# Kernel optimization log

Measured on AMD Instinct MI355X. Metric: run time of the kernel, lower is better.

Reference implementation:

```python
import jax, jax.numpy as jnp
import numpy as np

B, T, C = 256, 512, 256
K = 8  # number of distinct phoneme classes used (indices into phoneme_inventory)
# weights dict {'aa':2.0,'ae':0.5,'ah':1.5,'ao':1.2,'aw':0.8}, rest default 1.0,
# materialized as a dense per-class-index weight vector:
WEIGHTS = np.ones(K, dtype=np.float32)
WEIGHTS[:5] = [2.0, 0.5, 1.5, 1.2, 0.8]


def setup_inputs() -> dict:
    key = jax.random.key(0)
    k1, k2 = jax.random.split(key)
    embeddings = jax.random.normal(k1, (B, T, C), dtype=jnp.float32)
    phonemes = jax.random.randint(k2, (B, T), 0, K, dtype=jnp.int64)
    weights = jnp.asarray(WEIGHTS)
    return {"embeddings": embeddings, "phonemes": phonemes, "weights": weights}


def reference(embeddings, phonemes, weights):
    Bs, Ts, Cs = embeddings.shape
    # F.normalize(p=2, dim=-1) with eps=1e-12
    norm = jnp.linalg.norm(embeddings, axis=-1, keepdims=True)
    emb = embeddings / jnp.maximum(norm, 1e-12)
    # all-pairs cosine similarity per timestep: [T, B, B]
    exp_sim = jnp.exp(jnp.einsum('itc,jtc->tij', emb, emb))
    eye = jnp.eye(Bs, dtype=bool)  # [B, B]
    p = phonemes.T  # [T, B]
    pos = (p[:, :, None] == p[:, None, :]) & ~eye  # [T, B, B]
    num = jnp.where(pos, exp_sim, 0.0).sum(-1)          # [T, B]
    den = jnp.where(~eye, exp_sim, 0.0).sum(-1)          # [T, B]
    per_sample = -jnp.log(num / (den + 1e-6))            # [T, B]
    # segment-mean per (timestep, class), then weighted mean over present classes
    oh = jax.nn.one_hot(p, weights.shape[0], dtype=per_sample.dtype)  # [T, B, K]
    counts = oh.sum(1)                                   # [T, K]
    sums = jnp.einsum('tb,tbk->tk', per_sample, oh)      # [T, K]
    present = counts > 0
    class_mean = sums / jnp.maximum(counts, 1.0)
    loss_t = jnp.where(present, class_mean * weights, 0.0).sum(-1) / present.sum(-1)
    return loss_t.mean()
```

## Files before the change

### kernel.cpp

```cpp
#include <hip/hip_runtime.h>

#define Bn 256
#define Tn 512
#define Cn 256
#define Kn 8

typedef __attribute__((ext_vector_type(4))) float f32x4;

__global__ __launch_bounds__(512, 4)
void tcon_k(const float* __restrict__ emb,
            const int* __restrict__ phon,
            const float* __restrict__ wts,
            float* __restrict__ out) {
    __shared__ __align__(16) unsigned char Esh[Bn * Bn];
    __shared__ float invn[Bn];
    __shared__ int   pcls[Bn];
    __shared__ float num_s[Bn], den_s[Bn];
    __shared__ float csum[Kn];
    __shared__ int   ccnt[Kn];

    const int t    = blockIdx.x;
    const int tid  = threadIdx.x;
    const int lane = tid & 63;
    const int wave = tid >> 6;
    const int i0   = wave * 32;

    const int q   = lane >> 4;
    const int l15 = lane & 15;
    const int e3  = l15 & 7;

    if (tid < Kn) { csum[tid] = 0.0f; ccnt[tid] = 0; }
    if (tid < Bn) pcls[tid] = phon[tid * Tn + t];

    #pragma unroll 4
    for (int it = 0; it < 16; ++it) {
        const int f   = tid + it * 512;
        const int row = f >> 5;
        const int b   = f & 31;
        const float4* p = (const float4*)(emb + ((size_t)row * Tn + t) * Cn);
        const float4 v0 = p[2 * b];
        const float4 v1 = p[2 * b + 1];
        int lo = __builtin_amdgcn_cvt_pk_fp8_f32(v0.x, v0.y, 0, false);
        lo     = __builtin_amdgcn_cvt_pk_fp8_f32(v0.z, v0.w, lo, true);
        int hi = __builtin_amdgcn_cvt_pk_fp8_f32(v1.x, v1.y, 0, false);
        hi     = __builtin_amdgcn_cvt_pk_fp8_f32(v1.z, v1.w, hi, true);
        const int qq = b & 3, kk = b >> 2, kp = kk >> 1;
        const int ad = row * 256 + ((((qq << 2) + kp) ^ (row & 7)) << 4)
                     + ((kk & 1) << 3);
        int2 pk; pk.x = lo; pk.y = hi;
        *(int2*)&Esh[ad] = pk;
    }
    __syncthreads();

    f32x4 acc[2][2];

#define COMPUTE_HALF(JB) do {                                                \
    _Pragma("unroll") for (int _m = 0; _m < 2; ++_m)                         \
    _Pragma("unroll") for (int _n = 0; _n < 2; ++_n)                         \
        acc[_m][_n] = (f32x4){0.f, 0.f, 0.f, 0.f};                           \
    _Pragma("unroll") for (int _kp = 0; _kp < 4; ++_kp) {                    \
        const int _sw = (((q << 2) + _kp) ^ e3) << 4;                        \
        ulonglong2 _a[2], _b[2];                                             \
        _Pragma("unroll") for (int _m = 0; _m < 2; ++_m)                     \
            _a[_m] = *(const ulonglong2*)&Esh[(i0 + _m * 16 + l15) * 256 + _sw]; \
        _Pragma("unroll") for (int _n = 0; _n < 2; ++_n)                     \
            _b[_n] = *(const ulonglong2*)&Esh[((JB) + _n * 16 + l15) * 256 + _sw]; \
        _Pragma("unroll") for (int _m = 0; _m < 2; ++_m)                     \
        _Pragma("unroll") for (int _n = 0; _n < 2; ++_n) {                   \
            acc[_m][_n] = __builtin_amdgcn_mfma_f32_16x16x32_fp8_fp8(        \
                (long)_a[_m].x, (long)_b[_n].x, acc[_m][_n], 0, 0, 0);       \
            acc[_m][_n] = __builtin_amdgcn_mfma_f32_16x16x32_fp8_fp8(        \
                (long)_a[_m].y, (long)_b[_n].y, acc[_m][_n], 0, 0, 0);       \
        }                                                                    \
    }                                                                        \
} while (0)

#define EPILOGUE(JB) do {                                                    \
    _Pragma("unroll") for (int _n = 0; _n < 2; ++_n) {                       \
        const int _j  = (JB) + _n * 16 + l15;                                \
        const int _pj = pcls[_j];                                            \
        const float _ij = invn[_j];                                          \
        _Pragma("unroll") for (int _m = 0; _m < 2; ++_m)                     \
        _Pragma("unroll") for (int _r = 0; _r < 4; ++_r) {                   \
            const int _e = _m * 4 + _r;                                      \
            const int _ir = i0 + _m * 16 + q * 4 + _r;                       \
            const float _ex = __expf(acc[_m][_n][_r] * inv_i[_e] * _ij);     \
            const bool _nd = (_ir != _j);                                    \
            den_p[_e] += _nd ? _ex : 0.0f;                                   \
            num_p[_e] += (_nd && (_pj == pi[_e])) ? _ex : 0.0f;              \
        }                                                                    \
    }                                                                        \
} while (0)

    COMPUTE_HALF(i0);
    #pragma unroll
    for (int r = 0; r < 4; ++r)
        if (l15 == q * 4 + r) {
            invn[i0 + l15]      = rsqrtf(fmaxf(acc[0][0][r], 1e-24f));
            invn[i0 + 16 + l15] = rsqrtf(fmaxf(acc[1][1][r], 1e-24f));
        }
    __syncthreads();

    float num_p[8], den_p[8], inv_i[8];
    int   pi[8];
    #pragma unroll
    for (int e = 0; e < 8; ++e) {
        const int irow = i0 + (e >> 2) * 16 + q * 4 + (e & 3);
        num_p[e] = 0.0f; den_p[e] = 0.0f;
        pi[e]    = pcls[irow];
        inv_i[e] = invn[irow];
    }

    EPILOGUE(i0);
    for (int k = 1; k < 8; ++k) {
        const int jb = (wave ^ k) * 32;
        COMPUTE_HALF(jb);
        EPILOGUE(jb);
    }

    #pragma unroll
    for (int e = 0; e < 8; ++e) {
        float n = num_p[e], d = den_p[e];
        #pragma unroll
        for (int m = 1; m <= 8; m <<= 1) {
            n += __shfl_xor(n, m, 64);
            d += __shfl_xor(d, m, 64);
        }
        if (l15 == e) {
            const int irow = i0 + (e >> 2) * 16 + q * 4 + (e & 3);
            num_s[irow] = n;
            den_s[irow] = d;
        }
    }
    __syncthreads();

    if (tid < Bn) {
        const float ps = __logf(den_s[tid] + 1e-6f) - __logf(num_s[tid]);
        atomicAdd(&csum[pcls[tid]], ps);
        atomicAdd(&ccnt[pcls[tid]], 1);
    }
    __syncthreads();

    if (tid == 0) {
        float accv = 0.0f; int np = 0;
        #pragma unroll
        for (int k = 0; k < Kn; ++k)
            if (ccnt[k] > 0) { accv += (csum[k] / (float)ccnt[k]) * wts[k]; ++np; }
        atomicAdd(out, (accv / (float)np) * (1.0f / (float)Tn));
    }
#undef COMPUTE_HALF
#undef EPILOGUE
}

extern "C" void kernel_launch(void* const* d_in, const int* in_sizes, int n_in,
                              void* d_out, int out_size, void* d_ws, size_t ws_size,
                              hipStream_t stream) {
    const float* emb  = (const float*)d_in[0];
    const int*   phon = (const int*)d_in[1];
    const float* wts  = (const float*)d_in[2];
    float*       out  = (float*)d_out;

    hipMemsetAsync(out, 0, sizeof(float), stream);
    tcon_k<<<Tn, 512, 0, stream>>>(emb, phon, wts, out);
}
```

Baseline: 207.3 us.

## Use 1024-thread blocks with 16-row wave tiles instead of 32-row

```diff
diff --git a/kernel.cpp b/kernel.cpp
--- a/kernel.cpp
+++ b/kernel.cpp
@@ -7,7 +7,7 @@
 
 typedef __attribute__((ext_vector_type(4))) float f32x4;
 
-__global__ __launch_bounds__(512, 4)
+__global__ __launch_bounds__(1024, 8)
 void tcon_k(const float* __restrict__ emb,
             const int* __restrict__ phon,
             const float* __restrict__ wts,
@@ -23,7 +23,8 @@
     const int tid  = threadIdx.x;
     const int lane = tid & 63;
     const int wave = tid >> 6;
-    const int i0   = wave * 32;
+    const int i0   = wave * 16;
+    const int g0   = wave >> 1;
 
     const int q   = lane >> 4;
     const int l15 = lane & 15;
@@ -33,8 +34,8 @@
     if (tid < Bn) pcls[tid] = phon[tid * Tn + t];
 
     #pragma unroll 4
-    for (int it = 0; it < 16; ++it) {
-        const int f   = tid + it * 512;
+    for (int it = 0; it < 8; ++it) {
+        const int f   = tid + it * 1024;
         const int row = f >> 5;
         const int b   = f & 31;
         const float4* p = (const float4*)(emb + ((size_t)row * Tn + t) * Cn);
@@ -52,25 +53,22 @@
     }
     __syncthreads();
 
-    f32x4 acc[2][2];
+    f32x4 acc[2];
 
-#define COMPUTE_HALF(JB) do {                                                \
-    _Pragma("unroll") for (int _m = 0; _m < 2; ++_m)                         \
-    _Pragma("unroll") for (int _n = 0; _n < 2; ++_n)                         \
-        acc[_m][_n] = (f32x4){0.f, 0.f, 0.f, 0.f};                           \
+#define COMPUTE_G(JB) do {                                                   \
+    acc[0] = (f32x4){0.f, 0.f, 0.f, 0.f};                                    \
+    acc[1] = (f32x4){0.f, 0.f, 0.f, 0.f};                                    \
     _Pragma("unroll") for (int _kp = 0; _kp < 4; ++_kp) {                    \
         const int _sw = (((q << 2) + _kp) ^ e3) << 4;                        \
-        ulonglong2 _a[2], _b[2];                                             \
-        _Pragma("unroll") for (int _m = 0; _m < 2; ++_m)                     \
-            _a[_m] = *(const ulonglong2*)&Esh[(i0 + _m * 16 + l15) * 256 + _sw]; \
+        const ulonglong2 _a = *(const ulonglong2*)&Esh[(i0 + l15) * 256 + _sw]; \
+        ulonglong2 _b[2];                                                    \
         _Pragma("unroll") for (int _n = 0; _n < 2; ++_n)                     \
             _b[_n] = *(const ulonglong2*)&Esh[((JB) + _n * 16 + l15) * 256 + _sw]; \
-        _Pragma("unroll") for (int _m = 0; _m < 2; ++_m)                     \
         _Pragma("unroll") for (int _n = 0; _n < 2; ++_n) {                   \
-            acc[_m][_n] = __builtin_amdgcn_mfma_f32_16x16x32_fp8_fp8(        \
-                (long)_a[_m].x, (long)_b[_n].x, acc[_m][_n], 0, 0, 0);       \
-            acc[_m][_n] = __builtin_amdgcn_mfma_f32_16x16x32_fp8_fp8(        \
-                (long)_a[_m].y, (long)_b[_n].y, acc[_m][_n], 0, 0, 0);       \
+            acc[_n] = __builtin_amdgcn_mfma_f32_16x16x32_fp8_fp8(            \
+                (long)_a.x, (long)_b[_n].x, acc[_n], 0, 0, 0);               \
+            acc[_n] = __builtin_amdgcn_mfma_f32_16x16x32_fp8_fp8(            \
+                (long)_a.y, (long)_b[_n].y, acc[_n], 0, 0, 0);               \
         }                                                                    \
     }                                                                        \
 } while (0)
@@ -80,46 +78,49 @@
         const int _j  = (JB) + _n * 16 + l15;                                \
         const int _pj = pcls[_j];                                            \
         const float _ij = invn[_j];                                          \
-        _Pragma("unroll") for (int _m = 0; _m < 2; ++_m)                     \
         _Pragma("unroll") for (int _r = 0; _r < 4; ++_r) {                   \
-            const int _e = _m * 4 + _r;                                      \
-            const int _ir = i0 + _m * 16 + q * 4 + _r;                       \
-            const float _ex = __expf(acc[_m][_n][_r] * inv_i[_e] * _ij);     \
+            const int _ir = i0 + q * 4 + _r;                                 \
+            const float _ex = __expf(acc[_n][_r] * inv_i[_r] * _ij);         \
             const bool _nd = (_ir != _j);                                    \
-            den_p[_e] += _nd ? _ex : 0.0f;                                   \
-            num_p[_e] += (_nd && (_pj == pi[_e])) ? _ex : 0.0f;              \
+            den_p[_r] += _nd ? _ex : 0.0f;                                   \
+            num_p[_r] += (_nd && (_pj == pi[_r])) ? _ex : 0.0f;              \
         }                                                                    \
     }                                                                        \
 } while (0)
 
-    COMPUTE_HALF(i0);
-    #pragma unroll
-    for (int r = 0; r < 4; ++r)
-        if (l15 == q * 4 + r) {
-            invn[i0 + l15]      = rsqrtf(fmaxf(acc[0][0][r], 1e-24f));
-            invn[i0 + 16 + l15] = rsqrtf(fmaxf(acc[1][1][r], 1e-24f));
-        }
+    COMPUTE_G(g0 * 32);
+    if ((wave & 1) == 0) {
+        #pragma unroll
+        for (int r = 0; r < 4; ++r)
+            if (l15 == q * 4 + r)
+                invn[i0 + l15] = rsqrtf(fmaxf(acc[0][r], 1e-24f));
+    } else {
+        #pragma unroll
+        for (int r = 0; r < 4; ++r)
+            if (l15 == q * 4 + r)
+                invn[i0 + l15] = rsqrtf(fmaxf(acc[1][r], 1e-24f));
+    }
     __syncthreads();
 
-    float num_p[8], den_p[8], inv_i[8];
-    int   pi[8];
+    float num_p[4], den_p[4], inv_i[4];
+    int   pi[4];
     #pragma unroll
-    for (int e = 0; e < 8; ++e) {
-        const int irow = i0 + (e >> 2) * 16 + q * 4 + (e & 3);
+    for (int e = 0; e < 4; ++e) {
+        const int irow = i0 + q * 4 + e;
         num_p[e] = 0.0f; den_p[e] = 0.0f;
         pi[e]    = pcls[irow];
         inv_i[e] = invn[irow];
     }
 
-    EPILOGUE(i0);
+    EPILOGUE(g0 * 32);
     for (int k = 1; k < 8; ++k) {
-        const int jb = (wave ^ k) * 32;
-        COMPUTE_HALF(jb);
+        const int jb = (g0 ^ k) * 32;
+        COMPUTE_G(jb);
         EPILOGUE(jb);
     }
 
     #pragma unroll
-    for (int e = 0; e < 8; ++e) {
+    for (int e = 0; e < 4; ++e) {
         float n = num_p[e], d = den_p[e];
         #pragma unroll
         for (int m = 1; m <= 8; m <<= 1) {
@@ -127,9 +128,8 @@
             d += __shfl_xor(d, m, 64);
         }
         if (l15 == e) {
-            const int irow = i0 + (e >> 2) * 16 + q * 4 + (e & 3);
-            num_s[irow] = n;
-            den_s[irow] = d;
+            num_s[i0 + q * 4 + e] = n;
+            den_s[i0 + q * 4 + e] = d;
         }
     }
     __syncthreads();
@@ -148,7 +148,7 @@
             if (ccnt[k] > 0) { accv += (csum[k] / (float)ccnt[k]) * wts[k]; ++np; }
         atomicAdd(out, (accv / (float)np) * (1.0f / (float)Tn));
     }
-#undef COMPUTE_HALF
+#undef COMPUTE_G
 #undef EPILOGUE
 }
 
@@ -161,5 +161,5 @@
     float*       out  = (float*)d_out;
 
     hipMemsetAsync(out, 0, sizeof(float), stream);
-    tcon_k<<<Tn, 512, 0, stream>>>(emb, phon, wts, out);
+    tcon_k<<<Tn, 1024, 0, stream>>>(emb, phon, wts, out);
 }
```

After: 358.1 us. 1.73x slower.

## Split into prepass that normalizes and packs fp8 tiles, then direct LDS-load matmul kernel

Applied to the files above, without the earlier changes.

```diff
diff --git a/kernel.cpp b/kernel.cpp
--- a/kernel.cpp
+++ b/kernel.cpp
@@ -6,13 +6,167 @@
 #define Kn 8
 
 typedef __attribute__((ext_vector_type(4))) float f32x4;
+typedef __attribute__((address_space(1))) const unsigned char g_u8;
+typedef __attribute__((address_space(3))) unsigned char l_u8;
+
 
 __global__ __launch_bounds__(512, 4)
-void tcon_k(const float* __restrict__ emb,
+void tcon_p(const float* __restrict__ emb, unsigned char* __restrict__ q8) {
+    const int tid  = threadIdx.x;
+    const int lane = tid & 63;
+    const int wave = tid >> 6;
+    const int R    = blockIdx.x * 8 + wave;
+    const int b    = R >> 9;
+    const int t    = R & (Tn - 1);
+
+    const float4 v = ((const float4*)(emb + (size_t)R * Cn))[lane];
+    float n2 = v.x * v.x + v.y * v.y + v.z * v.z + v.w * v.w;
+    #pragma unroll
+    for (int m = 1; m <= 32; m <<= 1) n2 += __shfl_xor(n2, m, 64);
+    const float inv = rsqrtf(fmaxf(n2, 1e-24f));
+
+    int pk = __builtin_amdgcn_cvt_pk_fp8_f32(v.x * inv, v.y * inv, 0, false);
+    pk     = __builtin_amdgcn_cvt_pk_fp8_f32(v.z * inv, v.w * inv, pk, true);
+
+    const int q  = (lane >> 1) & 3;
+    const int kp = lane >> 4;
+    const int h  = (lane >> 3) & 1;
+    const int u  = ((q << 2) + kp) ^ (b & 7);
+    const size_t ad = (size_t)t * (Bn * Cn) + b * 256 + u * 16 + h * 8
+                    + (lane & 1) * 4;
+    *(int*)&q8[ad] = pk;
+}
+
+__global__ __launch_bounds__(512, 4)
+void tcon_m(const unsigned char* __restrict__ q8,
             const int* __restrict__ phon,
             const float* __restrict__ wts,
             float* __restrict__ out) {
-    __shared__ __align__(16) unsigned char Esh[Bn * Bn];
+    __shared__ __align__(16) unsigned char Esh[Bn * Cn];
+    __shared__ int   pcls[Bn];
+    __shared__ float num_s[Bn], den_s[Bn];
+    __shared__ float csum[Kn];
+    __shared__ int   ccnt[Kn];
+
+    const int t    = blockIdx.x;
+    const int tid  = threadIdx.x;
+    const int lane = tid & 63;
+    const int wave = tid >> 6;
+    const int i0   = wave * 32;
+
+    const int q   = lane >> 4;
+    const int l15 = lane & 15;
+    const int e3  = l15 & 7;
+
+    if (tid < Kn) { csum[tid] = 0.0f; ccnt[tid] = 0; }
+    if (tid < Bn) pcls[tid] = phon[tid * Tn + t];
+
+    {
+        const unsigned char* gt = q8 + (size_t)t * (Bn * Cn);
+        #pragma unroll
+        for (int i = 0; i < 8; ++i) {
+            __builtin_amdgcn_global_load_lds(
+                (g_u8*)(gt + wave * 8192 + i * 1024 + lane * 16),
+                (l_u8*)&Esh[wave * 8192 + i * 1024],
+                16, 0, 0);
+        }
+    }
+    __syncthreads();
+
+    f32x4 acc[2][2];
+
+#define COMPUTE_HALF(JB) do {                                                \
+    _Pragma("unroll") for (int _m = 0; _m < 2; ++_m)                         \
+    _Pragma("unroll") for (int _n = 0; _n < 2; ++_n)                         \
+        acc[_m][_n] = (f32x4){0.f, 0.f, 0.f, 0.f};                           \
+    _Pragma("unroll") for (int _kp = 0; _kp < 4; ++_kp) {                    \
+        const int _sw = (((q << 2) + _kp) ^ e3) << 4;                        \
+        ulonglong2 _a[2], _b[2];                                             \
+        _Pragma("unroll") for (int _m = 0; _m < 2; ++_m)                     \
+            _a[_m] = *(const ulonglong2*)&Esh[(i0 + _m * 16 + l15) * 256 + _sw]; \
+        _Pragma("unroll") for (int _n = 0; _n < 2; ++_n)                     \
+            _b[_n] = *(const ulonglong2*)&Esh[((JB) + _n * 16 + l15) * 256 + _sw]; \
+        _Pragma("unroll") for (int _m = 0; _m < 2; ++_m)                     \
+        _Pragma("unroll") for (int _n = 0; _n < 2; ++_n) {                   \
+            acc[_m][_n] = __builtin_amdgcn_mfma_f32_16x16x32_fp8_fp8(        \
+                (long)_a[_m].x, (long)_b[_n].x, acc[_m][_n], 0, 0, 0);       \
+            acc[_m][_n] = __builtin_amdgcn_mfma_f32_16x16x32_fp8_fp8(        \
+                (long)_a[_m].y, (long)_b[_n].y, acc[_m][_n], 0, 0, 0);       \
+        }                                                                    \
+    }                                                                        \
+} while (0)
+
+#define EPILOGUE(JB) do {                                                    \
+    _Pragma("unroll") for (int _n = 0; _n < 2; ++_n) {                       \
+        const int _j  = (JB) + _n * 16 + l15;                                \
+        const int _pj = pcls[_j];                                            \
+        _Pragma("unroll") for (int _m = 0; _m < 2; ++_m)                     \
+        _Pragma("unroll") for (int _r = 0; _r < 4; ++_r) {                   \
+            const int _e = _m * 4 + _r;                                      \
+            const int _ir = i0 + _m * 16 + q * 4 + _r;                       \
+            const float _ex = __expf(acc[_m][_n][_r]);                       \
+            const bool _nd = (_ir != _j);                                    \
+            den_p[_e] += _nd ? _ex : 0.0f;                                   \
+            num_p[_e] += (_nd && (_pj == pi[_e])) ? _ex : 0.0f;              \
+        }                                                                    \
+    }                                                                        \
+} while (0)
+
+    float num_p[8], den_p[8];
+    int   pi[8];
+    #pragma unroll
+    for (int e = 0; e < 8; ++e) {
+        const int irow = i0 + (e >> 2) * 16 + q * 4 + (e & 3);
+        num_p[e] = 0.0f; den_p[e] = 0.0f;
+        pi[e]    = pcls[irow];
+    }
+
+    for (int k = 0; k < 8; ++k) {
+        const int jb = (wave ^ k) * 32;
+        COMPUTE_HALF(jb);
+        EPILOGUE(jb);
+    }
+
+    #pragma unroll
+    for (int e = 0; e < 8; ++e) {
+        float n = num_p[e], d = den_p[e];
+        #pragma unroll
+        for (int m = 1; m <= 8; m <<= 1) {
+            n += __shfl_xor(n, m, 64);
+            d += __shfl_xor(d, m, 64);
+        }
+        if (l15 == e) {
+            const int irow = i0 + (e >> 2) * 16 + q * 4 + (e & 3);
+            num_s[irow] = n;
+            den_s[irow] = d;
+        }
+    }
+    __syncthreads();
+
+    if (tid < Bn) {
+        const float ps = __logf(den_s[tid] + 1e-6f) - __logf(num_s[tid]);
+        atomicAdd(&csum[pcls[tid]], ps);
+        atomicAdd(&ccnt[pcls[tid]], 1);
+    }
+    __syncthreads();
+
+    if (tid == 0) {
+        float accv = 0.0f; int np = 0;
+        #pragma unroll
+        for (int k = 0; k < Kn; ++k)
+            if (ccnt[k] > 0) { accv += (csum[k] / (float)ccnt[k]) * wts[k]; ++np; }
+        atomicAdd(out, (accv / (float)np) * (1.0f / (float)Tn));
+    }
+#undef COMPUTE_HALF
+#undef EPILOGUE
+}
+
+__global__ __launch_bounds__(512, 4)
+void tcon_f(const float* __restrict__ emb,
+            const int* __restrict__ phon,
+            const float* __restrict__ wts,
+            float* __restrict__ out) {
+    __shared__ __align__(16) unsigned char Esh[Bn * Cn];
     __shared__ float invn[Bn];
     __shared__ int   pcls[Bn];
     __shared__ float num_s[Bn], den_s[Bn];
@@ -161,5 +315,13 @@
     float*       out  = (float*)d_out;
 
     hipMemsetAsync(out, 0, sizeof(float), stream);
-    tcon_k<<<Tn, 512, 0, stream>>>(emb, phon, wts, out);
+
+    const size_t need = (size_t)Tn * Bn * Cn;
+    if (d_ws != nullptr && ws_size >= need) {
+        unsigned char* q8 = (unsigned char*)d_ws;
+        tcon_p<<<(Bn * Tn) / 8, 512, 0, stream>>>(emb, q8);
+        tcon_m<<<Tn, 512, 0, stream>>>(q8, phon, wts, out);
+    } else {
+        tcon_f<<<Tn, 512, 0, stream>>>(emb, phon, wts, out);
+    }
 }
```

Result: slower. 212.9 us (+2.7%).
